# Optimization experiments

Measured on AMD Instinct MI355X. Metric: run time of the kernel, lower is better.

Reference implementation:

```python
import jax, jax.numpy as jnp
import numpy as np

B, S, D = 4, 2048, 1024
H, DH = 16, 64


def setup_inputs() -> dict:
    key = jax.random.key(0)
    ks = jax.random.split(key, 5)
    x = jax.random.normal(ks[0], (B, S, D), dtype=jnp.float32)
    # causal mask: True where attention is disallowed (j > i)
    mask = jnp.triu(jnp.ones((S, S), dtype=bool), k=1)
    mask = jnp.broadcast_to(mask, (B, S, S))
    scale = 1.0 / np.sqrt(D)
    w_q = jax.random.normal(ks[1], (D, D), dtype=jnp.float32) * scale
    w_k = jax.random.normal(ks[2], (D, D), dtype=jnp.float32) * scale
    w_v = jax.random.normal(ks[3], (D, D), dtype=jnp.float32) * scale
    w_o = jax.random.normal(ks[4], (D, D), dtype=jnp.float32) * scale
    return {"x": x, "mask": mask, "w_q": w_q, "w_k": w_k, "w_v": w_v, "w_o": w_o}


def reference(x, mask, w_q, w_k, w_v, w_o):
    # torch Linear: y = x @ W.T (bias=False)
    b, s, d = x.shape
    q = (x @ w_q.T).reshape(b, s, H, DH).transpose(0, 2, 1, 3)  # [B,H,S,DH]
    k = (x @ w_k.T).reshape(b, s, H, DH).transpose(0, 2, 1, 3)
    v = (x @ w_v.T).reshape(b, s, H, DH).transpose(0, 2, 1, 3)
    inv_sqrt_dh = jnp.asarray(1.0 / np.sqrt(DH), dtype=x.dtype)
    scores = jnp.einsum('bhqd,bhkd->bhqk', q * inv_sqrt_dh, k)  # [B,H,S,S]
    scores = jnp.where(mask[:, None, :, :], -jnp.inf, scores)
    attn = jax.nn.softmax(scores, axis=-1)  # dropout is identity in eval mode
    out = jnp.einsum('bhqk,bhkd->bhqd', attn, v)  # [B,H,S,DH]
    out = out.transpose(0, 2, 1, 3).reshape(b, s, d)
    out = out @ w_o.T
    return out, attn
```

## Files before the change

### kernel.cpp

```cpp
#include <hip/hip_runtime.h>

#define DEV __device__ __forceinline__

typedef __attribute__((ext_vector_type(8))) short short8;
typedef __attribute__((ext_vector_type(4))) float f32x4;

DEV unsigned short f2bf(float f) {
  unsigned u = __builtin_bit_cast(unsigned, f);
  u += 0x7fff + ((u >> 16) & 1);
  return (unsigned short)(u >> 16);
}

DEV void gload_lds16(const void* g, void* l) {
  __builtin_amdgcn_global_load_lds(
      (const __attribute__((address_space(1))) void*)g,
      (__attribute__((address_space(3))) void*)l, 16, 0, 0);
}

#if __has_builtin(__builtin_amdgcn_exp2f)
#define EXP2F(x) __builtin_amdgcn_exp2f(x)
#else
#define EXP2F(x) exp2f(x)
#endif

#define LOG2E 1.4426950408889634f
#define QSCALE (0.125f * LOG2E)
#define MFMA16(a, b, c) __builtin_amdgcn_mfma_f32_16x16x32_bf16((a), (b), (c), 0, 0, 0)

__global__ void cvt_all(const float* __restrict__ x,
                        const float* __restrict__ w0, const float* __restrict__ w1,
                        const float* __restrict__ w2, const float* __restrict__ w3,
                        unsigned short* __restrict__ xb,
                        unsigned short* __restrict__ o0, unsigned short* __restrict__ o1,
                        unsigned short* __restrict__ o2, unsigned short* __restrict__ o3) {
  int i = blockIdx.x * blockDim.x + threadIdx.x;
  const float* in;
  unsigned short* out;
  int j;
  if (i < 2097152) {
    in = x; out = xb; j = i;
  } else {
    int k = i - 2097152;
    int sel = k >> 18; j = k & 0x3ffff;
    in  = sel == 0 ? w0 : sel == 1 ? w1 : sel == 2 ? w2 : w3;
    out = sel == 0 ? o0 : sel == 1 ? o1 : sel == 2 ? o2 : o3;
  }
  float4 v = ((const float4*)in)[j];
  ushort4 o;
  o.x = f2bf(v.x); o.y = f2bf(v.y); o.z = f2bf(v.z); o.w = f2bf(v.w);
  ((ushort4*)out)[j] = o;
}

#define GK 1024
template <int MODE>
DEV void gemm_body(const unsigned short* A, const unsigned short* Bw, void* Cout,
                   int bx, int by) {
  __shared__ unsigned short Ash[128 * 32];
  __shared__ unsigned short Bsh[128 * 32];
  const int tid = threadIdx.x;
  const int lane = tid & 63;
  const int w = tid >> 6;
  const int wm = w >> 1, wn = w & 1;
  const int l15 = lane & 15, l4 = lane >> 4;
  const int row0 = by * 128;
  const int col0 = bx * 128;

  f32x4 acc[4][4] = {};

  for (int kt = 0; kt < GK; kt += 32) {
    __syncthreads();
#pragma unroll
    for (int c = 0; c < 2; ++c) {
      int o = c * 4096 + tid * 16;
      int ldsoff = c * 4096 + w * 1024;
      int row = o >> 6, colb = o & 63;
      gload_lds16((const char*)A + (size_t)(row0 + row) * 2048 + kt * 2 + colb,
                  (char*)Ash + ldsoff);
      gload_lds16((const char*)Bw + (size_t)(col0 + row) * 2048 + kt * 2 + colb,
                  (char*)Bsh + ldsoff);
    }
    __syncthreads();
    short8 af[4], bf[4];
#pragma unroll
    for (int m = 0; m < 4; ++m)
      af[m] = *(const short8*)((const char*)Ash + (wm * 64 + m * 16 + l15) * 64 + l4 * 16);
#pragma unroll
    for (int n = 0; n < 4; ++n)
      bf[n] = *(const short8*)((const char*)Bsh + (wn * 64 + n * 16 + l15) * 64 + l4 * 16);
#pragma unroll
    for (int m = 0; m < 4; ++m)
#pragma unroll
      for (int n = 0; n < 4; ++n)
        acc[m][n] = MFMA16(af[m], bf[n], acc[m][n]);
  }

#pragma unroll
  for (int m = 0; m < 4; ++m)
#pragma unroll
    for (int n = 0; n < 4; ++n)
#pragma unroll
      for (int r = 0; r < 4; ++r) {
        int mrow = row0 + wm * 64 + m * 16 + l4 * 4 + r;
        int ncol = col0 + wn * 64 + n * 16 + l15;
        float v = acc[m][n][r];
        if (MODE == 0) {
          ((unsigned short*)Cout)[(size_t)mrow * 1024 + ncol] = f2bf(v);
        } else if (MODE == 1) {
          int b = mrow >> 11, s = mrow & 2047, h = ncol >> 6, d = ncol & 63;
          ((unsigned short*)Cout)[((size_t)((b * 16 + h) * 64 + d)) * 2048 + s] = f2bf(v);
        } else if (MODE == 2) {
          ((float*)Cout)[(size_t)mrow * 1024 + ncol] = v;
        } else {
          ((unsigned short*)Cout)[(size_t)mrow * 1024 + ncol] = f2bf(v * QSCALE);
        }
      }
}

__global__ __launch_bounds__(256) void gemm_qkv(const unsigned short* __restrict__ A,
                                                const unsigned short* __restrict__ Wq,
                                                const unsigned short* __restrict__ Wk,
                                                const unsigned short* __restrict__ Wv,
                                                unsigned short* __restrict__ Qo,
                                                unsigned short* __restrict__ Ko,
                                                unsigned short* __restrict__ Vto) {
  const int z = blockIdx.z;
  if (z == 0)      gemm_body<3>(A, Wq, Qo,  blockIdx.x, blockIdx.y);
  else if (z == 1) gemm_body<0>(A, Wk, Ko,  blockIdx.x, blockIdx.y);
  else             gemm_body<1>(A, Wv, Vto, blockIdx.x, blockIdx.y);
}

__global__ __launch_bounds__(256) void gemm_out(const unsigned short* __restrict__ A,
                                                const unsigned short* __restrict__ Bw,
                                                float* __restrict__ Cout) {
  gemm_body<2>(A, Bw, Cout, blockIdx.x, blockIdx.y);
}


DEV void stage_tile(const unsigned short* src_base, size_t row_stride, int col0,
                    char* ldsbase, int tid) {
  const int w = tid >> 6;
  const int r0 = tid >> 3;
  const int c0 = (tid & 7) ^ (r0 & 7);
  gload_lds16((const char*)(src_base + (size_t)r0 * row_stride + col0 + c0 * 8),
              ldsbase + w * 1024);
  const int r1 = 32 + r0;
  gload_lds16((const char*)(src_base + (size_t)r1 * row_stride + col0 + c0 * 8),
              ldsbase + 4096 + w * 1024);
}

__global__ __launch_bounds__(256, 4) void attn_fused(const unsigned short* __restrict__ Q,
                                                     const unsigned short* __restrict__ Kb,
                                                     const unsigned short* __restrict__ Vt,
                                                     float* __restrict__ attn,
                                                     unsigned short* __restrict__ O) {
  __shared__ char lds[40960];

  const int tid = threadIdx.x, lane = tid & 63, w = tid >> 6;
  const int l15 = lane & 15, l4 = lane >> 4;
  const int s7 = l15 & 7;
  const int off0 = (l4 ^ s7) << 4;
  const int off1 = ((l4 + 4) ^ s7) << 4;
  const int F = blockIdx.x;
  const int xcd = F & 7, slot = F >> 3;
  const int g = slot >> 4, r = slot & 15;
  const int pr = ((g >> 1) & 1) ? (15 - r) : r;
  const int bh = xcd + (g << 3);
  const int b = bh >> 4, h = bh & 15;

  const int qt0 = pr, qt1 = 31 - pr;
  const int q00 = qt0 * 64 + w * 16, q01 = qt1 * 64 + w * 16;
  const int myq0 = q00 + l15, myq1 = q01 + l15;

  const size_t qk_base = ((size_t)b * 2048) * 1024 + h * 64;
  const unsigned short* Qp = Q + qk_base;
  const unsigned short* Kp = Kb + qk_base;
  const unsigned short* Vp = Vt + (size_t)bh * 64 * 2048;
  float* Ap = attn + (size_t)bh * 2048 * 2048;
  char* pbase = lds + 32768 + w * 2048;

  float inv_l0, inv_l1;
  {
    short8 qf0[2], qf1[2];
    {
      const char* qrow0 = (const char*)(Qp + (size_t)myq0 * 1024);
      qf0[0] = *(const short8*)(qrow0 + (l4 * 8) * 2);
      qf0[1] = *(const short8*)(qrow0 + (32 + l4 * 8) * 2);
      const char* qrow1 = (const char*)(Qp + (size_t)myq1 * 1024);
      qf1[0] = *(const short8*)(qrow1 + (l4 * 8) * 2);
      qf1[1] = *(const short8*)(qrow1 + (32 + l4 * 8) * 2);
    }
    float lacc0[4] = {0.f, 0.f, 0.f, 0.f};
    float lacc1[4] = {0.f, 0.f, 0.f, 0.f};
    stage_tile(Kp, 1024, 0, lds, tid);
    stage_tile(Kp + (size_t)64 * 1024, 1024, 0, lds + 8192, tid);
    __syncthreads();
    const int nst = (qt1 + 2) >> 1;
    for (int st = 0; st < nst; ++st) {
      char* kbb = lds + (st & 1) * 16384;
      const int jt0 = 2 * st;
      if (jt0 + 2 <= qt1) {
        char* nb = lds + ((st + 1) & 1) * 16384;
        stage_tile(Kp + (size_t)(jt0 + 2) * 64 * 1024, 1024, 0, nb, tid);
        if (jt0 + 3 <= qt1)
          stage_tile(Kp + (size_t)(jt0 + 3) * 64 * 1024, 1024, 0, nb + 8192, tid);
      }
#pragma unroll
      for (int u = 0; u < 2; ++u) {
        const int jt = jt0 + u;
        if (jt > qt1) break;
        const char* kb = kbb + u * 8192;
        const int jbase = jt * 64;
        const bool diag1 = (jt == qt1);
        const bool do0 = (jt <= qt0);
        const bool diag0 = (jt == qt0);
#pragma unroll
        for (int jb = 0; jb < 4; ++jb) {
          const char* krow = kb + (jb * 16 + l15) * 128;
          short8 k0 = *(const short8*)(krow + off0);
          short8 k1 = *(const short8*)(krow + off1);
          f32x4 a1 = {};
          a1 = MFMA16(k0, qf1[0], a1);
          a1 = MFMA16(k1, qf1[1], a1);
#pragma unroll
          for (int rr = 0; rr < 4; ++rr) {
            int j = jbase + jb * 16 + l4 * 4 + rr;
            float e = EXP2F(a1[rr]);
            lacc1[rr] += (diag1 && j > myq1) ? 0.f : e;
          }
          if (do0) {
            f32x4 a0 = {};
            a0 = MFMA16(k0, qf0[0], a0);
            a0 = MFMA16(k1, qf0[1], a0);
#pragma unroll
            for (int rr = 0; rr < 4; ++rr) {
              int j = jbase + jb * 16 + l4 * 4 + rr;
              float e = EXP2F(a0[rr]);
              lacc0[rr] += (diag0 && j > myq0) ? 0.f : e;
            }
          }
        }
      }
      __syncthreads();
    }
    float lsum0 = (lacc0[0] + lacc0[1]) + (lacc0[2] + lacc0[3]);
    lsum0 += __shfl_xor(lsum0, 16);
    lsum0 += __shfl_xor(lsum0, 32);
    float lsum1 = (lacc1[0] + lacc1[1]) + (lacc1[2] + lacc1[3]);
    lsum1 += __shfl_xor(lsum1, 16);
    lsum1 += __shfl_xor(lsum1, 32);
    inv_l0 = 1.f / lsum0;
    inv_l1 = 1.f / lsum1;
  }

  for (int t = 0; t < 2; ++t) {
    const int qt = t ? qt1 : qt0;
    const float inv_l = t ? inv_l1 : inv_l0;
    const int q0 = qt * 64 + w * 16;
    const int myq = q0 + l15;

    short8 qf[2];
    {
      const char* qrow = (const char*)(Qp + (size_t)myq * 1024);
      qf[0] = *(const short8*)(qrow + (l4 * 8) * 2);
      qf[1] = *(const short8*)(qrow + (32 + l4 * 8) * 2);
    }

    f32x4 oacc[4] = {};
    stage_tile(Kp, 1024, 0, lds, tid);
    stage_tile(Vp, 2048, 0, lds + 16384, tid);
    __syncthreads();
    for (int jt = 0; jt <= qt; ++jt) {
      const char* kb = lds + (jt & 1) * 8192;
      const char* vb = lds + 16384 + (jt & 1) * 8192;
      if (jt < qt) {
        stage_tile(Kp + (size_t)(jt + 1) * 64 * 1024, 1024, 0,
                   lds + ((jt + 1) & 1) * 8192, tid);
        stage_tile(Vp, 2048, (jt + 1) * 64, lds + 16384 + ((jt + 1) & 1) * 8192, tid);
      }
      const int jbase = jt * 64;
      const bool diag = (jt == qt);
      float p[16];
#pragma unroll
      for (int jb = 0; jb < 4; ++jb) {
        const char* krow = kb + (jb * 16 + l15) * 128;
        short8 k0 = *(const short8*)(krow + off0);
        short8 k1 = *(const short8*)(krow + off1);
        f32x4 a = {};
        a = MFMA16(k0, qf[0], a);
        a = MFMA16(k1, qf[1], a);
#pragma unroll
        for (int rr = 0; rr < 4; ++rr) {
          int j = jbase + jb * 16 + l4 * 4 + rr;
          float e = EXP2F(a[rr]) * inv_l;
          p[jb * 4 + rr] = (diag && j > myq) ? 0.f : e;
        }
      }
#pragma unroll
      for (int jb = 0; jb < 4; ++jb) {
        unsigned u0 = f2bf(p[jb * 4]) | ((unsigned)f2bf(p[jb * 4 + 1]) << 16);
        unsigned u1 = f2bf(p[jb * 4 + 2]) | ((unsigned)f2bf(p[jb * 4 + 3]) << 16);
        uint2 uu; uu.x = u0; uu.y = u1;
        int slotw = (jb * 2 + (l4 >> 1)) ^ s7;
        *(uint2*)(pbase + l15 * 128 + slotw * 16 + (l4 & 1) * 8) = uu;
      }
#pragma unroll
      for (int ri = 0; ri < 4; ++ri) {
        int qrow = ri * 4 + l4;
        uint2 uu = *(const uint2*)(pbase + qrow * 128 +
                                   (((l15 >> 1) ^ (qrow & 7)) << 4) + (l15 & 1) * 8);
        f32x4 pv;
        pv[0] = __builtin_bit_cast(float, uu.x << 16);
        pv[1] = __builtin_bit_cast(float, uu.x & 0xffff0000u);
        pv[2] = __builtin_bit_cast(float, uu.y << 16);
        pv[3] = __builtin_bit_cast(float, uu.y & 0xffff0000u);
        *(f32x4*)(Ap + (size_t)(q0 + qrow) * 2048 + jbase + l15 * 4) = pv;
      }
      short8 pa0 = *(const short8*)(pbase + l15 * 128 + ((l4 ^ s7) << 4));
      short8 pa1 = *(const short8*)(pbase + l15 * 128 + (((4 + l4) ^ s7) << 4));
#pragma unroll
      for (int db = 0; db < 4; ++db) {
        const char* vrow = vb + (db * 16 + l15) * 128;
        short8 v0 = *(const short8*)(vrow + off0);
        short8 v1 = *(const short8*)(vrow + off1);
        oacc[db] = MFMA16(pa0, v0, oacc[db]);
        oacc[db] = MFMA16(pa1, v1, oacc[db]);
      }
      __syncthreads();
    }

    {
      f32x4 z = {};
      for (int jt = qt + 1; jt < 32; ++jt) {
        const int jbase = jt * 64;
#pragma unroll
        for (int ri = 0; ri < 4; ++ri) {
          int row = q0 + ri * 4 + l4;
          *(f32x4*)(Ap + (size_t)row * 2048 + jbase + l15 * 4) = z;
        }
      }
    }

#pragma unroll
    for (int db = 0; db < 4; ++db)
#pragma unroll
      for (int rr = 0; rr < 4; ++rr) {
        int q = q0 + l4 * 4 + rr;
        int d = db * 16 + l15;
        O[((size_t)b * 2048 + q) * 1024 + h * 64 + d] = f2bf(oacc[db][rr]);
      }
  }
}

extern "C" void kernel_launch(void* const* d_in, const int* in_sizes, int n_in,
                              void* d_out, int out_size, void* d_ws, size_t ws_size,
                              hipStream_t stream) {
  const float* x  = (const float*)d_in[0];
  const float* wq = (const float*)d_in[2];
  const float* wk = (const float*)d_in[3];
  const float* wv = (const float*)d_in[4];
  const float* wo = (const float*)d_in[5];

  float* out  = (float*)d_out;
  float* attn = out + (size_t)8192 * 1024;

  char* ws = (char*)d_ws;
  const size_t MB = 1 << 20;
  unsigned short* xb  = (unsigned short*)(ws);
  unsigned short* wqb = (unsigned short*)(ws + 16 * MB);
  unsigned short* wkb = (unsigned short*)(ws + 18 * MB);
  unsigned short* wvb = (unsigned short*)(ws + 20 * MB);
  unsigned short* wob = (unsigned short*)(ws + 22 * MB);
  unsigned short* Qb  = (unsigned short*)(ws + 24 * MB);
  unsigned short* Kb  = (unsigned short*)(ws + 40 * MB);
  unsigned short* Vtb = (unsigned short*)(ws + 56 * MB);
  unsigned short* Ob  = (unsigned short*)(ws + 72 * MB);

  cvt_all<<<12288, 256, 0, stream>>>(x, wq, wk, wv, wo, xb, wqb, wkb, wvb, wob);

  gemm_qkv<<<dim3(8, 64, 3), 256, 0, stream>>>(xb, wqb, wkb, wvb, Qb, Kb, Vtb);

  attn_fused<<<1024, 256, 0, stream>>>(Qb, Kb, Vtb, attn, Ob);

  gemm_out<<<dim3(8, 64), 256, 0, stream>>>(Ob, wob, out);
}
```

Measured before the change: 397.6 us.

## Merge two query tiles' second pass into one shared K/V stream loop

The second (normalized output) pass used to loop separately over the two paired query tiles, staging K and V from global memory twice. It now runs one loop over key tiles up to the later query tile and applies each staged K/V tile to both query tiles, the earlier one only while its causal range lasts. This cuts global-to-LDS staging traffic and barriers in that pass. In exchange it keeps two output accumulators and both Q fragments live, which raises register pressure under launch_bounds(256,4), and the reused per-wave P scratch buffer serializes the two tiles' work within a step.

```diff
diff --git a/kernel.cpp b/kernel.cpp
--- a/kernel.cpp
+++ b/kernel.cpp
@@ -148,6 +148,60 @@
               ldsbase + 4096 + w * 1024);
 }
 
+DEV void tile_work(const char* kb, const char* vb, char* pbase,
+                   const short8 qf[2], float inv_l, int jbase, bool diag,
+                   int q0, int myq, float* Ap, f32x4 oacc[4],
+                   int l15, int l4, int s7, int off0, int off1) {
+#pragma unroll
+  for (int jb = 0; jb < 4; ++jb) {
+    const char* krow = kb + (jb * 16 + l15) * 128;
+    short8 k0 = *(const short8*)(krow + off0);
+    short8 k1 = *(const short8*)(krow + off1);
+    f32x4 a = {};
+    a = MFMA16(k0, qf[0], a);
+    a = MFMA16(k1, qf[1], a);
+    float p0, p1, p2, p3;
+    {
+      int j = jbase + jb * 16 + l4 * 4;
+      float e0 = EXP2F(a[0]) * inv_l;
+      float e1 = EXP2F(a[1]) * inv_l;
+      float e2 = EXP2F(a[2]) * inv_l;
+      float e3 = EXP2F(a[3]) * inv_l;
+      p0 = (diag && j + 0 > myq) ? 0.f : e0;
+      p1 = (diag && j + 1 > myq) ? 0.f : e1;
+      p2 = (diag && j + 2 > myq) ? 0.f : e2;
+      p3 = (diag && j + 3 > myq) ? 0.f : e3;
+    }
+    unsigned u0 = f2bf(p0) | ((unsigned)f2bf(p1) << 16);
+    unsigned u1 = f2bf(p2) | ((unsigned)f2bf(p3) << 16);
+    uint2 uu; uu.x = u0; uu.y = u1;
+    int slotw = (jb * 2 + (l4 >> 1)) ^ s7;
+    *(uint2*)(pbase + l15 * 128 + slotw * 16 + (l4 & 1) * 8) = uu;
+  }
+#pragma unroll
+  for (int ri = 0; ri < 4; ++ri) {
+    int qrow = ri * 4 + l4;
+    uint2 uu = *(const uint2*)(pbase + qrow * 128 +
+                               (((l15 >> 1) ^ (qrow & 7)) << 4) + (l15 & 1) * 8);
+    f32x4 pv;
+    pv[0] = __builtin_bit_cast(float, uu.x << 16);
+    pv[1] = __builtin_bit_cast(float, uu.x & 0xffff0000u);
+    pv[2] = __builtin_bit_cast(float, uu.y << 16);
+    pv[3] = __builtin_bit_cast(float, uu.y & 0xffff0000u);
+    *(f32x4*)(Ap + (size_t)(q0 + qrow) * 2048 + jbase + l15 * 4) = pv;
+  }
+  short8 pa0 = *(const short8*)(pbase + l15 * 128 + ((l4 ^ s7) << 4));
+  short8 pa1 = *(const short8*)(pbase + l15 * 128 + (((4 + l4) ^ s7) << 4));
+#pragma unroll
+  for (int db = 0; db < 4; ++db) {
+    const char* vrow = vb + (db * 16 + l15) * 128;
+    short8 v0 = *(const short8*)(vrow + off0);
+    short8 v1 = *(const short8*)(vrow + off1);
+    oacc[db] = MFMA16(pa0, v0, oacc[db]);
+    oacc[db] = MFMA16(pa1, v1, oacc[db]);
+  }
+}
+
 __global__ __launch_bounds__(256, 4) void attn_fused(const unsigned short* __restrict__ Q,
                                                      const unsigned short* __restrict__ Kb,
                                                      const unsigned short* __restrict__ Vt,
@@ -178,17 +232,18 @@
   float* Ap = attn + (size_t)bh * 2048 * 2048;
   char* pbase = lds + 32768 + w * 2048;
 
+  short8 qf0[2], qf1[2];
+  {
+    const char* qrow0 = (const char*)(Qp + (size_t)myq0 * 1024);
+    qf0[0] = *(const short8*)(qrow0 + (l4 * 8) * 2);
+    qf0[1] = *(const short8*)(qrow0 + (32 + l4 * 8) * 2);
+    const char* qrow1 = (const char*)(Qp + (size_t)myq1 * 1024);
+    qf1[0] = *(const short8*)(qrow1 + (l4 * 8) * 2);
+    qf1[1] = *(const short8*)(qrow1 + (32 + l4 * 8) * 2);
+  }
+
   float inv_l0, inv_l1;
   {
-    short8 qf0[2], qf1[2];
-    {
-      const char* qrow0 = (const char*)(Qp + (size_t)myq0 * 1024);
-      qf0[0] = *(const short8*)(qrow0 + (l4 * 8) * 2);
-      qf0[1] = *(const short8*)(qrow0 + (32 + l4 * 8) * 2);
-      const char* qrow1 = (const char*)(Qp + (size_t)myq1 * 1024);
-      qf1[0] = *(const short8*)(qrow1 + (l4 * 8) * 2);
-      qf1[1] = *(const short8*)(qrow1 + (32 + l4 * 8) * 2);
-    }
     float lacc0[4] = {0.f, 0.f, 0.f, 0.f};
     float lacc1[4] = {0.f, 0.f, 0.f, 0.f};
     stage_tile(Kp, 1024, 0, lds, tid);
@@ -252,103 +307,58 @@
     inv_l1 = 1.f / lsum1;
   }
 
-  for (int t = 0; t < 2; ++t) {
-    const int qt = t ? qt1 : qt0;
-    const float inv_l = t ? inv_l1 : inv_l0;
-    const int q0 = qt * 64 + w * 16;
-    const int myq = q0 + l15;
-
-    short8 qf[2];
-    {
-      const char* qrow = (const char*)(Qp + (size_t)myq * 1024);
-      qf[0] = *(const short8*)(qrow + (l4 * 8) * 2);
-      qf[1] = *(const short8*)(qrow + (32 + l4 * 8) * 2);
-    }
-
-    f32x4 oacc[4] = {};
-    stage_tile(Kp, 1024, 0, lds, tid);
-    stage_tile(Vp, 2048, 0, lds + 16384, tid);
+  f32x4 oacc0[4] = {};
+  f32x4 oacc1[4] = {};
+  stage_tile(Kp, 1024, 0, lds, tid);
+  stage_tile(Vp, 2048, 0, lds + 16384, tid);
+  __syncthreads();
+  for (int jt = 0; jt <= qt1; ++jt) {
+    const char* kb = lds + (jt & 1) * 8192;
+    const char* vb = lds + 16384 + (jt & 1) * 8192;
+    if (jt < qt1) {
+      stage_tile(Kp + (size_t)(jt + 1) * 64 * 1024, 1024, 0,
+                 lds + ((jt + 1) & 1) * 8192, tid);
+      stage_tile(Vp, 2048, (jt + 1) * 64, lds + 16384 + ((jt + 1) & 1) * 8192, tid);
+    }
+    const int jbase = jt * 64;
+    tile_work(kb, vb, pbase, qf1, inv_l1, jbase, jt == qt1, q01, myq1, Ap, oacc1,
+              l15, l4, s7, off0, off1);
+    if (jt <= qt0)
+      tile_work(kb, vb, pbase, qf0, inv_l0, jbase, jt == qt0, q00, myq0, Ap, oacc0,
+                l15, l4, s7, off0, off1);
     __syncthreads();
-    for (int jt = 0; jt <= qt; ++jt) {
-      const char* kb = lds + (jt & 1) * 8192;
-      const char* vb = lds + 16384 + (jt & 1) * 8192;
-      if (jt < qt) {
-        stage_tile(Kp + (size_t)(jt + 1) * 64 * 1024, 1024, 0,
-                   lds + ((jt + 1) & 1) * 8192, tid);
-        stage_tile(Vp, 2048, (jt + 1) * 64, lds + 16384 + ((jt + 1) & 1) * 8192, tid);
-      }
+  }
+
+  {
+    f32x4 z = {};
+    for (int jt = qt0 + 1; jt < 32; ++jt) {
       const int jbase = jt * 64;
-      const bool diag = (jt == qt);
-      float p[16];
-#pragma unroll
-      for (int jb = 0; jb < 4; ++jb) {
-        const char* krow = kb + (jb * 16 + l15) * 128;
-        short8 k0 = *(const short8*)(krow + off0);
-        short8 k1 = *(const short8*)(krow + off1);
-        f32x4 a = {};
-        a = MFMA16(k0, qf[0], a);
-        a = MFMA16(k1, qf[1], a);
-#pragma unroll
-        for (int rr = 0; rr < 4; ++rr) {
-          int j = jbase + jb * 16 + l4 * 4 + rr;
-          float e = EXP2F(a[rr]) * inv_l;
-          p[jb * 4 + rr] = (diag && j > myq) ? 0.f : e;
-        }
-      }
-#pragma unroll
-      for (int jb = 0; jb < 4; ++jb) {
-        unsigned u0 = f2bf(p[jb * 4]) | ((unsigned)f2bf(p[jb * 4 + 1]) << 16);
-        unsigned u1 = f2bf(p[jb * 4 + 2]) | ((unsigned)f2bf(p[jb * 4 + 3]) << 16);
-        uint2 uu; uu.x = u0; uu.y = u1;
-        int slotw = (jb * 2 + (l4 >> 1)) ^ s7;
-        *(uint2*)(pbase + l15 * 128 + slotw * 16 + (l4 & 1) * 8) = uu;
-      }
 #pragma unroll
       for (int ri = 0; ri < 4; ++ri) {
-        int qrow = ri * 4 + l4;
-        uint2 uu = *(const uint2*)(pbase + qrow * 128 +
-                                   (((l15 >> 1) ^ (qrow & 7)) << 4) + (l15 & 1) * 8);
-        f32x4 pv;
-        pv[0] = __builtin_bit_cast(float, uu.x << 16);
-        pv[1] = __builtin_bit_cast(float, uu.x & 0xffff0000u);
-        pv[2] = __builtin_bit_cast(float, uu.y << 16);
-        pv[3] = __builtin_bit_cast(float, uu.y & 0xffff0000u);
-        *(f32x4*)(Ap + (size_t)(q0 + qrow) * 2048 + jbase + l15 * 4) = pv;
-      }
-      short8 pa0 = *(const short8*)(pbase + l15 * 128 + ((l4 ^ s7) << 4));
-      short8 pa1 = *(const short8*)(pbase + l15 * 128 + (((4 + l4) ^ s7) << 4));
-#pragma unroll
-      for (int db = 0; db < 4; ++db) {
-        const char* vrow = vb + (db * 16 + l15) * 128;
-        short8 v0 = *(const short8*)(vrow + off0);
-        short8 v1 = *(const short8*)(vrow + off1);
-        oacc[db] = MFMA16(pa0, v0, oacc[db]);
-        oacc[db] = MFMA16(pa1, v1, oacc[db]);
-      }
-      __syncthreads();
-    }
-
-    {
-      f32x4 z = {};
-      for (int jt = qt + 1; jt < 32; ++jt) {
-        const int jbase = jt * 64;
-#pragma unroll
-        for (int ri = 0; ri < 4; ++ri) {
-          int row = q0 + ri * 4 + l4;
-          *(f32x4*)(Ap + (size_t)row * 2048 + jbase + l15 * 4) = z;
-        }
-      }
-    }
-
-#pragma unroll
-    for (int db = 0; db < 4; ++db)
-#pragma unroll
-      for (int rr = 0; rr < 4; ++rr) {
-        int q = q0 + l4 * 4 + rr;
-        int d = db * 16 + l15;
-        O[((size_t)b * 2048 + q) * 1024 + h * 64 + d] = f2bf(oacc[db][rr]);
-      }
-  }
+        int row = q00 + ri * 4 + l4;
+        *(f32x4*)(Ap + (size_t)row * 2048 + jbase + l15 * 4) = z;
+      }
+    }
+    for (int jt = qt1 + 1; jt < 32; ++jt) {
+      const int jbase = jt * 64;
+#pragma unroll
+      for (int ri = 0; ri < 4; ++ri) {
+        int row = q01 + ri * 4 + l4;
+        *(f32x4*)(Ap + (size_t)row * 2048 + jbase + l15 * 4) = z;
+      }
+    }
+  }
+
+#pragma unroll
+  for (int db = 0; db < 4; ++db)
+#pragma unroll
+    for (int rr = 0; rr < 4; ++rr) {
+      int d = db * 16 + l15;
+      int qa = q00 + l4 * 4 + rr;
+      O[((size_t)b * 2048 + qa) * 1024 + h * 64 + d] = f2bf(oacc0[db][rr]);
+      int qb2 = q01 + l4 * 4 + rr;
+      O[((size_t)b * 2048 + qb2) * 1024 + h * 64 + d] = f2bf(oacc1[db][rr]);
+    }
 }
 
 extern "C" void kernel_launch(void* const* d_in, const int* in_sizes, int n_in,
```

Result: slower. 540.4 us (+35.9%).
